# Optimization experiments

Measured on AMD Instinct MI355X. Metric: run time of the kernel, lower is better.

The kernel has to match this reference:

```python
import jax, jax.numpy as jnp
import numpy as np

N = 10000          # nodes
E = 160000         # edges
T = 32             # seq_len == n_timesteps
H = 256            # hidden_size
K = 4              # edge_embedding_dim
NF = T * 6         # node_features
PRED = 8           # predicted_timesteps
T_TEACH = T - PRED # teacher-forced steps


def setup_inputs() -> dict:
    key = jax.random.key(0)
    ks = jax.random.split(key, 16)
    s = 0.05
    return {
        "x": jax.random.normal(ks[0], (N, NF), jnp.float32),
        "edge_index": jax.random.randint(ks[1], (2, E), 0, N, jnp.int64),
        "z": jax.random.uniform(ks[2], (E, K), jnp.float32),
        # inner f_out: Linear(H, NF) + ReLU
        "Wf": jax.random.normal(ks[3], (H, NF), jnp.float32) * s,
        "bf": jax.random.normal(ks[4], (NF,), jnp.float32) * s,
        # k-1 edge MLPs: Linear(2*NF, H) -> ReLU -> Linear(H, H), stacked
        "W1": jax.random.normal(ks[5], (K - 1, 2 * NF, H), jnp.float32) * s,
        "b1": jax.random.normal(ks[6], (K - 1, H), jnp.float32) * s,
        "W2": jax.random.normal(ks[7], (K - 1, H, H), jnp.float32) * s,
        "b2": jax.random.normal(ks[8], (K - 1, H), jnp.float32) * s,
        # GRUCell(6, H): torch gate order r, z, n
        "Wih": jax.random.normal(ks[9], (3 * H, 6), jnp.float32) * s,
        "bih": jax.random.normal(ks[10], (3 * H,), jnp.float32) * s,
        "Whh": jax.random.normal(ks[11], (3 * H, H), jnp.float32) * s,
        "bhh": jax.random.normal(ks[12], (3 * H,), jnp.float32) * s,
        # outer f_out: Linear(H, 6) + ReLU
        "Wo": jax.random.normal(ks[13], (H, 6), jnp.float32) * s,
        "bo": jax.random.normal(ks[14], (6,), jnp.float32) * s,
    }


def _forward(x, edge_index, z, Wf, bf, W1, b1, W2, b2, Wih, bih, Whh, bhh, Wo, bo):
    src = edge_index[0]  # x_j (source)
    dst = edge_index[1]  # x_i (target, aggregation index)
    zw = z[:, 1:K].T[:, :, None]  # [K-1, E, 1]
    ones_e = jnp.ones((E,), x.dtype)
    cnt = jnp.maximum(jax.ops.segment_sum(ones_e, dst, num_segments=N), 1.0)[:, None]

    def step(carry, inp):
        h, prev = carry
        t, x_t = inp
        inputs = jnp.where(t < T_TEACH, x_t, prev)  # [N, 6]
        fh = jax.nn.relu(h @ Wf + bf)               # [N, NF]
        # message: cat([x_i, x_j]) = [target, source], detached in torch
        ef = jax.lax.stop_gradient(
            jnp.concatenate([fh[dst], fh[src]], axis=1))  # [E, 2*NF]
        h1 = jax.nn.relu(jnp.einsum('ef,kfh->keh', ef, W1) + b1[:, None, :])
        h2 = jnp.einsum('keh,khg->keg', h1, W2) + b2[:, None, :]  # [K-1,E,H]
        msg = jnp.sum(zw * h2, axis=0)              # [E, H]
        m = jax.ops.segment_sum(msg, dst, num_segments=N) / cnt  # scatter-mean
        # GRUCell(inputs, hidden=m)
        gx = inputs @ Wih.T + bih                   # [N, 3H]
        gh = m @ Whh.T + bhh                        # [N, 3H]
        rx, zx, nx = jnp.split(gx, 3, axis=1)
        rh, zh, nh = jnp.split(gh, 3, axis=1)
        r = jax.nn.sigmoid(rx + rh)
        zg = jax.nn.sigmoid(zx + zh)
        n = jnp.tanh(nx + r * nh)
        h_new = (1.0 - zg) * n + zg * m             # [N, H]
        mu = inputs + jax.nn.relu(h_new @ Wo + bo)  # [N, 6]
        return (h_new, mu), mu

    x_seq = x.reshape(N, T, 6).transpose(1, 0, 2)   # [T, N, 6]
    ts = jnp.arange(T)
    h0 = jnp.zeros((N, H), x.dtype)
    p0 = jnp.zeros((N, 6), x.dtype)
    _, mus = jax.lax.scan(step, (h0, p0), (ts, x_seq))  # [T, N, 6]
    return mus.transpose(1, 0, 2).reshape(N, NF)


def reference(x, edge_index, z, Wf, bf, W1, b1, W2, b2, Wih, bih, Whh, bhh, Wo, bo):
    return _forward(x, edge_index, z, Wf, bf, W1, b1, W2, b2,
                    Wih, bih, Whh, bhh, Wo, bo)
```

## Files before the change

kernel.cpp:

```cpp
#include <hip/hip_runtime.h>
#include <hip/hip_bf16.h>

#define NN 10000
#define NE 160000
#define TS 32
#define HID 256
#define NFEAT 192
#define TTEACH 24

typedef unsigned short u16;
typedef unsigned int u32;
typedef __attribute__((ext_vector_type(8))) short bf16x8;
typedef __attribute__((ext_vector_type(4))) float f32x4;

__device__ __forceinline__ float bf2f(u16 u){
    u32 v = ((u32)u) << 16;
    union { u32 i; float f; } c; c.i = v; return c.f;
}
__device__ __forceinline__ u16 f2bf(float f){
    union { float f; u32 i; } c; c.f = f;
    u32 i = c.i;
    u32 lsb = (i >> 16) & 1u;
    i += 0x7fffu + lsb;
    return (u16)(i >> 16);
}

__global__ void fill_f32(float* p, float v, int n){
    int i = blockIdx.x * 256 + threadIdx.x;
    if (i < n) p[i] = v;
}
__global__ void fill_i32(int* p, int v, int n){
    int i = blockIdx.x * 256 + threadIdx.x;
    if (i < n) p[i] = v;
}
__global__ void copy_i32(const int* __restrict__ a, int* __restrict__ b, int n){
    int i = blockIdx.x * 256 + threadIdx.x;
    if (i < n) b[i] = a[i];
}
__global__ void copy_f32(const float* __restrict__ a, float* __restrict__ b, int n){
    int i = blockIdx.x * 256 + threadIdx.x;
    if (i < n) b[i] = a[i];
}

__global__ void detect_f32(const u16* __restrict__ zraw, int* __restrict__ flag){
    int c = 0;
    for (int i = 0; i < 128; i++) if (zraw[2*i] >= 0x4000) c++;
    *flag = (c > 8) ? 1 : 0;
}
__global__ void conv_f32(const void* __restrict__ in, float* __restrict__ outp,
                         int n, const int* __restrict__ flag){
    int i = blockIdx.x * 256 + threadIdx.x;
    if (i >= n) return;
    if (*flag) outp[i] = ((const float*)in)[i];
    else       outp[i] = bf2f(((const u16*)in)[i]);
}
__global__ void detect_i64(const int* __restrict__ ei_raw, int* __restrict__ flag){
    int zz = 0;
    #pragma unroll
    for (int i = 0; i < 32; i++) zz |= ei_raw[2*i + 1];
    *flag = (zz == 0) ? 1 : 0;
}
__global__ void copy_edges(const int* __restrict__ ei_raw, const int* __restrict__ flag,
                           int* __restrict__ src, int* __restrict__ dst){
    int e = blockIdx.x * 256 + threadIdx.x;
    if (e >= NE) return;
    int st = (*flag) ? 2 : 1;
    src[e] = ei_raw[(size_t)e * st];
    dst[e] = ei_raw[((size_t)NE + e) * st];
}

__global__ void degree_k(const int* __restrict__ dst, int* __restrict__ cnt, int n){
    int e = blockIdx.x * 256 + threadIdx.x;
    if (e < n) atomicAdd(&cnt[dst[e]], 1);
}
__global__ void invcnt_k(const int* __restrict__ cnt, float* __restrict__ inv, int n){
    int i = blockIdx.x * 256 + threadIdx.x;
    if (i < n) inv[i] = 1.0f / fmaxf((float)cnt[i], 1.0f);
}

__global__ void scan_k(const int* __restrict__ cnt, int* __restrict__ binoff){
    __shared__ int ps[1024];
    int t = threadIdx.x;
    int s = 0;
    if (t < 1000)
        for (int i = 0; i < 10; i++) s += cnt[t*10 + i];
    ps[t] = s;
    __syncthreads();
    for (int ofs = 1; ofs < 1024; ofs <<= 1){
        int v = (t >= ofs) ? ps[t - ofs] : 0;
        __syncthreads();
        ps[t] += v;
        __syncthreads();
    }
    if (t < 1000){
        int run = (t == 0) ? 0 : ps[t-1];
        for (int i = 0; i < 10; i++){
            binoff[t*10 + i] = run;
            run += cnt[t*10 + i];
        }
    }
}
__global__ void scatter_k(const int* __restrict__ src32, const int* __restrict__ dst32,
                          const float* __restrict__ zc, int* __restrict__ cur,
                          int* __restrict__ srcS, int* __restrict__ dstS,
                          float* __restrict__ zS){
    int e = blockIdx.x * 256 + threadIdx.x;
    if (e >= NE) return;
    int d = dst32[e];
    int pos = atomicAdd(&cur[d], 1);
    srcS[pos] = src32[e];
    dstS[pos] = d;
    zS[pos]        = zc[(size_t)e*4 + 1];
    zS[NE + pos]   = zc[(size_t)e*4 + 2];
    zS[2*NE + pos] = zc[(size_t)e*4 + 3];
}

__global__ void zsum_k(const int* __restrict__ dst32, const float* __restrict__ zc,
                       float* __restrict__ zsum){
    int e = blockIdx.x * 256 + threadIdx.x;
    if (e >= NE) return;
    int d = dst32[e];
    atomicAdd(&zsum[d*3 + 0], zc[(size_t)e*4 + 1]);
    atomicAdd(&zsum[d*3 + 1], zc[(size_t)e*4 + 2]);
    atomicAdd(&zsum[d*3 + 2], zc[(size_t)e*4 + 3]);
}
__global__ void build_bias_k(const float* __restrict__ zsum, const float* __restrict__ b2c,
                             float* __restrict__ bias_node){
    int idx = blockIdx.x * 256 + threadIdx.x;
    if (idx >= NN * 256) return;
    int n = idx >> 8, c = idx & 255;
    bias_node[idx] = zsum[n*3]*b2c[c] + zsum[n*3+1]*b2c[256+c] + zsum[n*3+2]*b2c[512+c];
}

__global__ void build_wft(const float* __restrict__ Wfc, u16* __restrict__ WfT){
    int idx = blockIdx.x * 256 + threadIdx.x;
    if (idx < 256 * 192){
        int k = idx / 192, n = idx % 192;
        WfT[(size_t)n * 256 + k] = f2bf(Wfc[idx]);
    }
}
__global__ void build_w1t(const float* __restrict__ W1c, u16* __restrict__ W1T){
    int idx = blockIdx.x * 256 + threadIdx.x;
    if (idx < 1536 * 192){
        int n = idx / 192, k = idx % 192;
        int kblk = n >> 9, part = (n >> 8) & 1, c = n & 255;
        W1T[idx] = f2bf(W1c[(size_t)kblk * (384*256) + (size_t)(part*192 + k) * 256 + c]);
    }
}
__global__ void conv_bf16(const float* __restrict__ in, u16* __restrict__ outp, int n){
    int i = blockIdx.x * 256 + threadIdx.x;
    if (i < n) outp[i] = f2bf(in[i]);
}
__global__ void build_w2t(const float* __restrict__ W2c, u16* __restrict__ W2T){
    int idx = blockIdx.x * 256 + threadIdx.x;
    if (idx < 768 * 256){
        int k = idx / 256, n = idx % 256;
        W2T[(size_t)n * 768 + k] = f2bf(W2c[idx]);
    }
}

template<int MODE>
__global__ __launch_bounds__(256, 2) void gemm_mfma(
    const u16* __restrict__ A16, const u16* __restrict__ BT16,
    const float* __restrict__ bias, float* __restrict__ Cf, u16* __restrict__ Cb,
    const float* __restrict__ A32, const float* __restrict__ rowscale,
    int M, int Kd, int Nd)
{
    __shared__ __align__(16) u16 Alds[256 * 40];
    __shared__ __align__(16) u16 Blds[64 * 40];
    const int tid = threadIdx.x;
    const int m0 = blockIdx.x * 256;
    const int n0 = blockIdx.y * 64;
    const int wave = tid >> 6, lane = tid & 63;
    const int quad = lane >> 4, l16 = lane & 15;

    const f32x4 zero4 = {0.f, 0.f, 0.f, 0.f};
    f32x4 acc[4][4];
    #pragma unroll
    for (int r=0;r<4;r++)
        #pragma unroll
        for (int c=0;c<4;c++) acc[r][c] = zero4;

    const int arow = m0 + tid;
    const u16* ap = (MODE == 2) ? nullptr : &A16[(size_t)arow * Kd];
    const int bn = tid >> 2, bseg = tid & 3;
    const u16* bp = &BT16[(size_t)(n0 + bn) * Kd + bseg * 8];
    float rs = 0.f;
    if (MODE == 2 && arow < M) rs = rowscale[arow];

    for (int k0 = 0; k0 < Kd; k0 += 32){
        if (MODE == 2){
            if (arow < M){
                const float4* q = reinterpret_cast<const float4*>(&A32[(size_t)arow * Kd + k0]);
                u32 pk[16];
                #pragma unroll
                for (int s=0;s<8;s++){
                    float4 v = q[s];
                    float2 p0; p0.x = v.x * rs; p0.y = v.y * rs;
                    float2 p1; p1.x = v.z * rs; p1.y = v.w * rs;
                    __hip_bfloat162 h0 = __float22bfloat162_rn(p0);
                    __hip_bfloat162 h1 = __float22bfloat162_rn(p1);
                    pk[2*s]   = *reinterpret_cast<u32*>(&h0);
                    pk[2*s+1] = *reinterpret_cast<u32*>(&h1);
                }
                #pragma unroll
                for (int s=0;s<4;s++)
                    *reinterpret_cast<uint4*>(&Alds[tid * 40 + s*8]) = *reinterpret_cast<uint4*>(&pk[4*s]);
            } else {
                uint4 zz = {0,0,0,0};
                #pragma unroll
                for (int s=0;s<4;s++)
                    *reinterpret_cast<uint4*>(&Alds[tid * 40 + s*8]) = zz;
            }
        } else {
            if (arow < M){
                const uint4* q = reinterpret_cast<const uint4*>(ap + k0);
                uint4 v0 = q[0], v1 = q[1], v2 = q[2], v3 = q[3];
                *reinterpret_cast<uint4*>(&Alds[tid * 40])      = v0;
                *reinterpret_cast<uint4*>(&Alds[tid * 40 + 8])  = v1;
                *reinterpret_cast<uint4*>(&Alds[tid * 40 + 16]) = v2;
                *reinterpret_cast<uint4*>(&Alds[tid * 40 + 24]) = v3;
            } else {
                uint4 zz = {0,0,0,0};
                #pragma unroll
                for (int s=0;s<4;s++)
                    *reinterpret_cast<uint4*>(&Alds[tid * 40 + s*8]) = zz;
            }
        }
        {
            uint4 v = *reinterpret_cast<const uint4*>(bp + k0);
            *reinterpret_cast<uint4*>(&Blds[bn * 40 + bseg * 8]) = v;
        }
        __syncthreads();
        bf16x8 af[4], bfr[4];
        #pragma unroll
        for (int r=0;r<4;r++)
            af[r] = *reinterpret_cast<const bf16x8*>(&Alds[(wave*64 + r*16 + l16) * 40 + quad * 8]);
        #pragma unroll
        for (int c=0;c<4;c++)
            bfr[c] = *reinterpret_cast<const bf16x8*>(&Blds[(c*16 + l16) * 40 + quad * 8]);
        #pragma unroll
        for (int r=0;r<4;r++)
            #pragma unroll
            for (int c=0;c<4;c++)
                acc[r][c] = __builtin_amdgcn_mfma_f32_16x16x32_bf16(af[r], bfr[c], acc[r][c], 0, 0, 0);
        __syncthreads();
    }
    #pragma unroll
    for (int c=0;c<4;c++){
        int col = n0 + c*16 + l16;
        float bv = 0.f;
        if (MODE == 0 || MODE == 2) bv = bias[col];
        if (MODE == 1){
            int part = (col >> 8) & 1;
            if (part == 0) bv = bias[(col >> 9) * 256 + (col & 255)];
        }
        #pragma unroll
        for (int r=0;r<4;r++){
            #pragma unroll
            for (int reg=0;reg<4;reg++){
                int row = m0 + wave*64 + r*16 + quad*4 + reg;
                if (row >= M) continue;
                float v = acc[r][c][reg] + bv;
                if (MODE == 0) v = fmaxf(v, 0.f);
                if (MODE == 2) Cf[(size_t)row * Nd + col] = v;
                else           Cb[(size_t)row * Nd + col] = f2bf(v);
            }
        }
    }
}

__global__ __launch_bounds__(256, 2) void edge_mfma(
    const u16* __restrict__ AB16, const u16* __restrict__ W2T,
    const float* __restrict__ zS,
    const int* __restrict__ srcS, const int* __restrict__ dstS,
    float* __restrict__ m_acc)
{
    __shared__ __align__(16) char smem[15360];
    u16*   Alds = (u16*)smem;
    u16*   Blds = (u16*)(smem + 5120);
    float* stg  = (float*)smem;
    __shared__ float zc3[3][64];
    __shared__ int dstc[64], srcc[64];
    const int tid = threadIdx.x;
    const int cb = blockIdx.x * 128;
    const int eb = blockIdx.y * 64;

    if (tid < 64){
        srcc[tid] = srcS[eb + tid];
        dstc[tid] = dstS[eb + tid];
    }
    int tz = tid - 64;
    if (tz >= 0 && tz < 192){
        int g = tz / 64, e = tz % 64;
        zc3[g][e] = zS[(size_t)g * NE + eb + e];
    }
    __syncthreads();

    const int wave = tid >> 6, lane = tid & 63;
    const int quad = lane >> 4, l16 = lane & 15;
    const int est = tid >> 2, seg = tid & 3;

    const f32x4 zero4 = {0.f, 0.f, 0.f, 0.f};
    f32x4 acc[4][2];
    #pragma unroll
    for (int r=0;r<4;r++)
        #pragma unroll
        for (int c=0;c<2;c++) acc[r][c] = zero4;

    const int d = dstc[est], s = srcc[est];
    const u16* paB = &AB16[(size_t)d * 1536];
    const u16* pbB = &AB16[(size_t)s * 1536 + 256];
    const u16* bwB = &W2T[(size_t)(cb + (tid >> 2)) * 768 + (tid & 3) * 8];

    uint4 pa = *reinterpret_cast<const uint4*>(&paB[seg * 8]);
    uint4 pb = *reinterpret_cast<const uint4*>(&pbB[seg * 8]);

    for (int kc = 0; kc < 768; kc += 32){
        const int g = kc >> 8;
        {
            union { uint4 v; u32 w[4]; } UA, UB;
            UA.v = pa; UB.v = pb;
            float zk = zc3[g][est];
            u32 pk[4];
            #pragma unroll
            for (int i=0;i<4;i++){
                float2 fa = __bfloat1622float2(*reinterpret_cast<__hip_bfloat162*>(&UA.w[i]));
                float2 fb = __bfloat1622float2(*reinterpret_cast<__hip_bfloat162*>(&UB.w[i]));
                float2 v;
                v.x = zk * fmaxf(fa.x + fb.x, 0.f);
                v.y = zk * fmaxf(fa.y + fb.y, 0.f);
                __hip_bfloat162 hr = __float22bfloat162_rn(v);
                pk[i] = *reinterpret_cast<u32*>(&hr);
            }
            *reinterpret_cast<uint4*>(&Alds[est * 40 + seg * 8]) = *reinterpret_cast<uint4*>(pk);
        }
        {
            uint4 w0 = *reinterpret_cast<const uint4*>(&bwB[kc]);
            uint4 w1 = *reinterpret_cast<const uint4*>(&bwB[(size_t)64 * 768 + kc]);
            *reinterpret_cast<uint4*>(&Blds[(tid >> 2) * 40 + (tid & 3) * 8]) = w0;
            *reinterpret_cast<uint4*>(&Blds[((tid >> 2) + 64) * 40 + (tid & 3) * 8]) = w1;
        }
        __syncthreads();
        if (kc + 32 < 768){
            const int kn = kc + 32;
            const int gn = kn >> 8;
            const int jn = (kn & 255) + seg * 8;
            pa = *reinterpret_cast<const uint4*>(&paB[gn * 512 + jn]);
            pb = *reinterpret_cast<const uint4*>(&pbB[gn * 512 + jn]);
        }
        bf16x8 af[4], bfr[2];
        #pragma unroll
        for (int r=0;r<4;r++)
            af[r] = *reinterpret_cast<const bf16x8*>(&Alds[(r*16 + l16) * 40 + quad * 8]);
        #pragma unroll
        for (int c=0;c<2;c++)
            bfr[c] = *reinterpret_cast<const bf16x8*>(&Blds[(wave*32 + c*16 + l16) * 40 + quad * 8]);
        #pragma unroll
        for (int r=0;r<4;r++)
            #pragma unroll
            for (int c=0;c<2;c++)
                acc[r][c] = __builtin_amdgcn_mfma_f32_16x16x32_bf16(af[r], bfr[c], acc[r][c], 0, 0, 0);
        __syncthreads();
    }
    const int colL = lane & 31;
    const int half = lane >> 5;
    const int colG = cb + wave*32 + colL;
    float sum = 0.f;
    int cur_d = -1;
    #pragma unroll
    for (int r = 0; r < 4; r++){
        #pragma unroll
        for (int c=0;c<2;c++)
            #pragma unroll
            for (int reg=0;reg<4;reg++)
                stg[wave*(16*33) + (quad*4 + reg)*33 + c*16 + l16] = acc[r][c][reg];
        __syncthreads();
        if ((r >> 1) == half){
            for (int e = 0; e < 16; e++){
                int eg = r*16 + e;
                int dn = dstc[eg];
                float v = stg[wave*(16*33) + e*33 + colL];
                if (dn != cur_d){
                    if (cur_d >= 0) atomicAdd(&m_acc[(size_t)cur_d * 256 + colG], sum);
                    cur_d = dn; sum = v;
                } else {
                    sum += v;
                }
            }
        }
        __syncthreads();
    }
    if (cur_d >= 0) atomicAdd(&m_acc[(size_t)cur_d * 256 + colG], sum);
}

__global__ void gates_mu_k(
    const float* __restrict__ gh, float* __restrict__ m_acc,
    const float* __restrict__ inv_cnt, const float* __restrict__ bias_node,
    const float* __restrict__ x,
    const float* __restrict__ Wih, const float* __restrict__ bih,
    const float* __restrict__ Wo, const float* __restrict__ bo,
    float* __restrict__ prev, u16* __restrict__ h16, void* __restrict__ out,
    const int* __restrict__ flag, int t)
{
    const int n = blockIdx.x;
    const int j = threadIdx.x;
    const int idx = n * 256 + j;
    float inp[6];
    if (t < TTEACH){
        #pragma unroll
        for (int c=0;c<6;c++) inp[c] = x[(size_t)n * NFEAT + t * 6 + c];
    } else {
        #pragma unroll
        for (int c=0;c<6;c++) inp[c] = prev[n * 6 + c];
    }
    float m = m_acc[idx] * inv_cnt[n];
    m_acc[idx] = bias_node[idx];
    float gxr = bih[j], gxz = bih[256 + j], gxn = bih[512 + j];
    #pragma unroll
    for (int c=0;c<6;c++){
        gxr += inp[c] * Wih[j * 6 + c];
        gxz += inp[c] * Wih[(256 + j) * 6 + c];
        gxn += inp[c] * Wih[(512 + j) * 6 + c];
    }
    float ghr = gh[(size_t)n * 768 + j];
    float ghz = gh[(size_t)n * 768 + 256 + j];
    float ghn = gh[(size_t)n * 768 + 512 + j];
    float r  = 1.f / (1.f + __expf(-(gxr + ghr)));
    float zg = 1.f / (1.f + __expf(-(gxz + ghz)));
    float nn = tanhf(gxn + r * ghn);
    float hv = (1.f - zg) * nn + zg * m;
    h16[idx] = f2bf(hv);
    __shared__ float hl[256];
    __shared__ float part[6][9];
    hl[j] = hv;
    __syncthreads();
    if (j < 48){
        int c = j >> 3, p = j & 7;
        float s = 0.f;
        #pragma unroll 8
        for (int q = 0; q < 32; q++){
            int jj = p*32 + q;
            s += hl[jj] * Wo[jj * 6 + c];
        }
        part[c][p] = s;
    }
    __syncthreads();
    if (j < 6){
        float s = bo[j];
        #pragma unroll
        for (int p = 0; p < 8; p++) s += part[j][p];
        float mu = inp[j] + fmaxf(s, 0.f);
        if (*flag) ((float*)out)[(size_t)n * NFEAT + t * 6 + j] = mu;
        else       ((u16*)out)[(size_t)n * NFEAT + t * 6 + j] = f2bf(mu);
        prev[n * 6 + j] = mu;
    }
}

extern "C" void kernel_launch(void* const* d_in, const int* in_sizes, int n_in,
                              void* d_out, int out_size, void* d_ws, size_t ws_size,
                              hipStream_t stream)
{
    const void* x_r   = d_in[0];
    const int*  ei    = (const int*)d_in[1];
    const void* z_r   = d_in[2];
    const void* Wf_r  = d_in[3];
    const void* bf_r  = d_in[4];
    const void* W1_r  = d_in[5];
    const void* b1_r  = d_in[6];
    const void* W2_r  = d_in[7];
    const void* b2_r  = d_in[8];
    const void* Wih_r = d_in[9];
    const void* bih_r = d_in[10];
    const void* Whh_r = d_in[11];
    const void* bhh_r = d_in[12];
    const void* Wo_r  = d_in[13];
    const void* bo_r  = d_in[14];

    char* ws = (char*)d_ws;
    size_t off = 0;
    auto alloc = [&](size_t bytes){
        void* p = ws + off;
        off += (bytes + 255) & ~(size_t)255;
        return p;
    };
    u16*   h16   = (u16*)  alloc((size_t)NN * HID * 2);
    float* prev  = (float*)alloc((size_t)NN * 6 * 4);
    u16*   fh16  = (u16*)  alloc((size_t)NN * NFEAT * 2);
    u16*   AB16  = (u16*)  alloc((size_t)NN * 1536 * 2);
    float* m_acc = (float*)alloc((size_t)NN * HID * 4);
    float* gh    = (float*)alloc((size_t)NN * 768 * 4);
    float* invc  = (float*)alloc((size_t)NN * 4);
    int*   cnt   = (int*)  alloc((size_t)NN * 4);
    int*   binoff= (int*)  alloc((size_t)(NN + 1) * 4);
    int*   curw  = (int*)  alloc((size_t)NN * 4);
    float* zsum  = (float*)alloc((size_t)NN * 3 * 4);
    float* biasN = (float*)alloc((size_t)NN * HID * 4);
    u16*   WfT   = (u16*)  alloc((size_t)192 * 256 * 2);
    u16*   W1T   = (u16*)  alloc((size_t)1536 * 192 * 2);
    u16*   Whh16 = (u16*)  alloc((size_t)768 * 256 * 2);
    u16*   W2T   = (u16*)  alloc((size_t)256 * 768 * 2);
    int*   src32 = (int*)  alloc((size_t)NE * 4);
    int*   dst32 = (int*)  alloc((size_t)NE * 4);
    int*   srcS  = (int*)  alloc((size_t)NE * 4);
    int*   dstS  = (int*)  alloc((size_t)NE * 4);
    float* zS    = (float*)alloc((size_t)3 * NE * 4);
    int*   fdt   = (int*)  alloc(256);
    int*   fidx  = (int*)  alloc(256);
    float* xc   = (float*)alloc((size_t)NN * NFEAT * 4);
    float* zc   = (float*)alloc((size_t)NE * 4 * 4);
    float* Wfc  = (float*)alloc((size_t)256 * 192 * 4);
    float* bfc  = (float*)alloc(192 * 4);
    float* W1c  = (float*)alloc((size_t)3 * 384 * 256 * 4);
    float* b1c  = (float*)alloc(768 * 4);
    float* W2c  = (float*)alloc((size_t)3 * 256 * 256 * 4);
    float* b2c  = (float*)alloc(768 * 4);
    float* Wihc = (float*)alloc((size_t)768 * 6 * 4);
    float* bihc = (float*)alloc(768 * 4);
    float* Whhc = (float*)alloc((size_t)768 * 256 * 4);
    float* bhhc = (float*)alloc(768 * 4);
    float* Woc  = (float*)alloc((size_t)256 * 6 * 4);
    float* boc  = (float*)alloc(6 * 4);

    detect_f32<<<1, 1, 0, stream>>>((const u16*)z_r, fdt);
    detect_i64<<<1, 1, 0, stream>>>(ei, fidx);
    copy_edges<<<(NE + 255)/256, 256, 0, stream>>>(ei, fidx, src32, dst32);

    auto conv = [&](const void* in, float* outp, int n){
        conv_f32<<<(n + 255)/256, 256, 0, stream>>>(in, outp, n, fdt);
    };
    conv(x_r,   xc,   NN * NFEAT);
    conv(z_r,   zc,   NE * 4);
    conv(Wf_r,  Wfc,  256 * 192);
    conv(bf_r,  bfc,  192);
    conv(W1_r,  W1c,  3 * 384 * 256);
    conv(b1_r,  b1c,  768);
    conv(W2_r,  W2c,  3 * 256 * 256);
    conv(b2_r,  b2c,  768);
    conv(Wih_r, Wihc, 768 * 6);
    conv(bih_r, bihc, 768);
    conv(Whh_r, Whhc, 768 * 256);
    conv(bhh_r, bhhc, 768);
    conv(Wo_r,  Woc,  256 * 6);
    conv(bo_r,  boc,  6);

    fill_f32<<<(NN*HID/2 + 255)/256, 256, 0, stream>>>((float*)h16, 0.f, NN*HID/2);
    fill_f32<<<(NN*6 + 255)/256, 256, 0, stream>>>(prev, 0.f, NN*6);
    fill_i32<<<(NN + 255)/256, 256, 0, stream>>>(cnt, 0, NN);
    fill_f32<<<(NN*3 + 255)/256, 256, 0, stream>>>(zsum, 0.f, NN*3);
    degree_k<<<(NE + 255)/256, 256, 0, stream>>>(dst32, cnt, NE);
    invcnt_k<<<(NN + 255)/256, 256, 0, stream>>>(cnt, invc, NN);
    zsum_k<<<(NE + 255)/256, 256, 0, stream>>>(dst32, zc, zsum);
    build_bias_k<<<(NN*HID + 255)/256, 256, 0, stream>>>(zsum, b2c, biasN);
    copy_f32<<<(NN*HID + 255)/256, 256, 0, stream>>>(biasN, m_acc, NN*HID);
    scan_k<<<1, 1024, 0, stream>>>(cnt, binoff);
    copy_i32<<<(NN + 255)/256, 256, 0, stream>>>(binoff, curw, NN);
    scatter_k<<<(NE + 255)/256, 256, 0, stream>>>(src32, dst32, zc, curw, srcS, dstS, zS);
    build_wft<<<(256*192 + 255)/256, 256, 0, stream>>>(Wfc, WfT);
    build_w1t<<<(1536*192 + 255)/256, 256, 0, stream>>>(W1c, W1T);
    conv_bf16<<<(768*256 + 255)/256, 256, 0, stream>>>(Whhc, Whh16, 768*256);
    build_w2t<<<(768*256 + 255)/256, 256, 0, stream>>>(W2c, W2T);

    for (int t = 0; t < TS; t++){
        gemm_mfma<0><<<dim3(40, 3), 256, 0, stream>>>(h16, WfT, bfc, nullptr, fh16, nullptr, nullptr, NN, 256, NFEAT);
        gemm_mfma<1><<<dim3(40, 24), 256, 0, stream>>>(fh16, W1T, b1c, nullptr, AB16, nullptr, nullptr, NN, NFEAT, 1536);
        edge_mfma<<<dim3(2, 2500), 256, 0, stream>>>(AB16, W2T, zS, srcS, dstS, m_acc);
        gemm_mfma<2><<<dim3(40, 12), 256, 0, stream>>>(nullptr, Whh16, bhhc, gh, nullptr, m_acc, invc, NN, 256, 768);
        gates_mu_k<<<NN, 256, 0, stream>>>(gh, m_acc, invc, biasN, xc, Wihc, bihc, Woc, boc, prev, h16, d_out, fdt, t);
    }
}
```

Before: 7.627 ms.

## Compute all 256 output columns per edge block to avoid recomputing edge activations

The edge kernel previously split the 256 output columns across two blocks, so each block re-gathered the source/target rows and recomputed the ReLU/z-scaled A tile. Now one block covers all 256 columns for its 64 edges, with each wave owning 64 columns and the accumulator tile growing to 4x4. This halves the gather and elementwise work and the number of blocks. In exchange it raises register and LDS use (accumulators and staging buffer), which may lower occupancy, and each block loads four weight rows per thread per k-step.

```diff
diff --git a/kernel.cpp b/kernel.cpp
--- a/kernel.cpp
+++ b/kernel.cpp
@@ -276,15 +276,14 @@
     const int* __restrict__ srcS, const int* __restrict__ dstS,
     float* __restrict__ m_acc)
 {
-    __shared__ __align__(16) char smem[15360];
+    __shared__ __align__(16) char smem[25600];
     u16*   Alds = (u16*)smem;
     u16*   Blds = (u16*)(smem + 5120);
     float* stg  = (float*)smem;
     __shared__ float zc3[3][64];
     __shared__ int dstc[64], srcc[64];
     const int tid = threadIdx.x;
-    const int cb = blockIdx.x * 128;
-    const int eb = blockIdx.y * 64;
+    const int eb = blockIdx.x * 64;
 
     if (tid < 64){
         srcc[tid] = srcS[eb + tid];
@@ -299,29 +298,31 @@
 
     const int wave = tid >> 6, lane = tid & 63;
     const int quad = lane >> 4, l16 = lane & 15;
-    const int est = tid >> 2, seg = tid & 3;
+    const int eA = tid & 63;
+    const int sg = tid >> 6;
 
     const f32x4 zero4 = {0.f, 0.f, 0.f, 0.f};
-    f32x4 acc[4][2];
+    f32x4 acc[4][4];
     #pragma unroll
     for (int r=0;r<4;r++)
         #pragma unroll
-        for (int c=0;c<2;c++) acc[r][c] = zero4;
-
-    const int d = dstc[est], s = srcc[est];
+        for (int c=0;c<4;c++) acc[r][c] = zero4;
+
+    const int d = dstc[eA], s = srcc[eA];
+    const float zk0 = zc3[0][eA], zk1 = zc3[1][eA], zk2 = zc3[2][eA];
     const u16* paB = &AB16[(size_t)d * 1536];
     const u16* pbB = &AB16[(size_t)s * 1536 + 256];
-    const u16* bwB = &W2T[(size_t)(cb + (tid >> 2)) * 768 + (tid & 3) * 8];
-
-    uint4 pa = *reinterpret_cast<const uint4*>(&paB[seg * 8]);
-    uint4 pb = *reinterpret_cast<const uint4*>(&pbB[seg * 8]);
+    const u16* bwB = &W2T[(size_t)eA * 768 + sg * 8];
+
+    uint4 pa = *reinterpret_cast<const uint4*>(&paB[sg * 8]);
+    uint4 pb = *reinterpret_cast<const uint4*>(&pbB[sg * 8]);
 
     for (int kc = 0; kc < 768; kc += 32){
         const int g = kc >> 8;
+        const float zk = (g == 0) ? zk0 : ((g == 1) ? zk1 : zk2);
         {
             union { uint4 v; u32 w[4]; } UA, UB;
             UA.v = pa; UB.v = pb;
-            float zk = zc3[g][est];
             u32 pk[4];
             #pragma unroll
             for (int i=0;i<4;i++){
@@ -333,65 +334,60 @@
                 __hip_bfloat162 hr = __float22bfloat162_rn(v);
                 pk[i] = *reinterpret_cast<u32*>(&hr);
             }
-            *reinterpret_cast<uint4*>(&Alds[est * 40 + seg * 8]) = *reinterpret_cast<uint4*>(pk);
-        }
-        {
-            uint4 w0 = *reinterpret_cast<const uint4*>(&bwB[kc]);
-            uint4 w1 = *reinterpret_cast<const uint4*>(&bwB[(size_t)64 * 768 + kc]);
-            *reinterpret_cast<uint4*>(&Blds[(tid >> 2) * 40 + (tid & 3) * 8]) = w0;
-            *reinterpret_cast<uint4*>(&Blds[((tid >> 2) + 64) * 40 + (tid & 3) * 8]) = w1;
+            *reinterpret_cast<uint4*>(&Alds[eA * 40 + sg * 8]) = *reinterpret_cast<uint4*>(pk);
+        }
+        #pragma unroll
+        for (int i=0;i<4;i++){
+            uint4 w = *reinterpret_cast<const uint4*>(&bwB[(size_t)i * 64 * 768 + kc]);
+            *reinterpret_cast<uint4*>(&Blds[(eA + i*64) * 40 + sg * 8]) = w;
         }
         __syncthreads();
         if (kc + 32 < 768){
             const int kn = kc + 32;
             const int gn = kn >> 8;
-            const int jn = (kn & 255) + seg * 8;
+            const int jn = (kn & 255) + sg * 8;
             pa = *reinterpret_cast<const uint4*>(&paB[gn * 512 + jn]);
             pb = *reinterpret_cast<const uint4*>(&pbB[gn * 512 + jn]);
         }
-        bf16x8 af[4], bfr[2];
+        bf16x8 af[4], bfr[4];
         #pragma unroll
         for (int r=0;r<4;r++)
             af[r] = *reinterpret_cast<const bf16x8*>(&Alds[(r*16 + l16) * 40 + quad * 8]);
         #pragma unroll
-        for (int c=0;c<2;c++)
-            bfr[c] = *reinterpret_cast<const bf16x8*>(&Blds[(wave*32 + c*16 + l16) * 40 + quad * 8]);
+        for (int c=0;c<4;c++)
+            bfr[c] = *reinterpret_cast<const bf16x8*>(&Blds[(wave*64 + c*16 + l16) * 40 + quad * 8]);
         #pragma unroll
         for (int r=0;r<4;r++)
             #pragma unroll
-            for (int c=0;c<2;c++)
+            for (int c=0;c<4;c++)
                 acc[r][c] = __builtin_amdgcn_mfma_f32_16x16x32_bf16(af[r], bfr[c], acc[r][c], 0, 0, 0);
         __syncthreads();
     }
-    const int colL = lane & 31;
-    const int half = lane >> 5;
-    const int colG = cb + wave*32 + colL;
     float sum = 0.f;
     int cur_d = -1;
+    const int colg = wave*64 + lane;
     #pragma unroll
     for (int r = 0; r < 4; r++){
         #pragma unroll
-        for (int c=0;c<2;c++)
+        for (int c=0;c<4;c++)
             #pragma unroll
             for (int reg=0;reg<4;reg++)
-                stg[wave*(16*33) + (quad*4 + reg)*33 + c*16 + l16] = acc[r][c][reg];
-        __syncthreads();
-        if ((r >> 1) == half){
-            for (int e = 0; e < 16; e++){
-                int eg = r*16 + e;
-                int dn = dstc[eg];
-                float v = stg[wave*(16*33) + e*33 + colL];
-                if (dn != cur_d){
-                    if (cur_d >= 0) atomicAdd(&m_acc[(size_t)cur_d * 256 + colG], sum);
-                    cur_d = dn; sum = v;
-                } else {
-                    sum += v;
-                }
+                stg[wave*(16*65) + (quad*4 + reg)*65 + c*16 + l16] = acc[r][c][reg];
+        __syncthreads();
+        for (int e = 0; e < 16; e++){
+            int eg = r*16 + e;
+            int dn = dstc[eg];
+            float v = stg[wave*(16*65) + e*65 + lane];
+            if (dn != cur_d){
+                if (cur_d >= 0) atomicAdd(&m_acc[(size_t)cur_d * 256 + colg], sum);
+                cur_d = dn; sum = v;
+            } else {
+                sum += v;
             }
         }
         __syncthreads();
     }
-    if (cur_d >= 0) atomicAdd(&m_acc[(size_t)cur_d * 256 + colG], sum);
+    if (cur_d >= 0) atomicAdd(&m_acc[(size_t)cur_d * 256 + colg], sum);
 }
 
 __global__ void gates_mu_k(
@@ -564,7 +560,7 @@
     for (int t = 0; t < TS; t++){
         gemm_mfma<0><<<dim3(40, 3), 256, 0, stream>>>(h16, WfT, bfc, nullptr, fh16, nullptr, nullptr, NN, 256, NFEAT);
         gemm_mfma<1><<<dim3(40, 24), 256, 0, stream>>>(fh16, W1T, b1c, nullptr, AB16, nullptr, nullptr, NN, NFEAT, 1536);
-        edge_mfma<<<dim3(2, 2500), 256, 0, stream>>>(AB16, W2T, zS, srcS, dstS, m_acc);
+        edge_mfma<<<2500, 256, 0, stream>>>(AB16, W2T, zS, srcS, dstS, m_acc);
         gemm_mfma<2><<<dim3(40, 12), 256, 0, stream>>>(nullptr, Whh16, bhhc, gh, nullptr, m_acc, invc, NN, 256, 768);
         gates_mu_k<<<NN, 256, 0, stream>>>(gh, m_acc, invc, biasN, xc, Wihc, bihc, Woc, boc, prev, h16, d_out, fdt, t);
     }
```

Measured after the change: 9.052 ms. 1.19x slower.
